# Kernel tuning notes

Hardware: AMD Instinct MI355X
Metric: run time of the kernel (lower is better)

The kernel has to match this reference:

```python
import jax, jax.numpy as jnp
import numpy as np

N = 16384      # total nodes (hits)
K = 8          # n_neighbors
NB = 8         # number of graphs in batch
IN_C = 6       # in_channels
HID = 128      # hidden_channels
NCLS = 3       # num_classes
SLOPE = 0.2    # GATv2 leaky_relu negative_slope
BIG = 1e30     # mask value for cross-graph pairs


def setup_inputs() -> dict:
    key = jax.random.key(0)
    ks = jax.random.split(key, 32)
    coord = jax.random.normal(ks[0], (N, 3), dtype=jnp.float32)
    feat = jax.random.normal(ks[1], (N, IN_C), dtype=jnp.float32)
    batch = jnp.sort(jax.random.randint(ks[2], (N,), 0, NB)).astype(jnp.int32)

    def lin_w(k, fan_in, fan_out):
        return (jax.random.normal(k, (fan_in, fan_out), dtype=jnp.float32)
                * np.float32(1.0 / np.sqrt(fan_in)))

    inp = {"coord": coord, "feat": feat, "batch": batch}
    dims = [IN_C, HID, HID]  # input dim of each of the 3 GATv2 layers
    kidx = 3
    for l, din in enumerate(dims):
        inp[f"Wl{l}"] = lin_w(ks[kidx], din, HID); kidx += 1
        inp[f"bl{l}"] = jnp.zeros((HID,), jnp.float32)
        inp[f"Wr{l}"] = lin_w(ks[kidx], din, HID); kidx += 1
        inp[f"br{l}"] = jnp.zeros((HID,), jnp.float32)
        inp[f"att{l}"] = (jax.random.normal(ks[kidx], (HID,), dtype=jnp.float32)
                          * np.float32(1.0 / np.sqrt(HID))); kidx += 1
        inp[f"bias{l}"] = jnp.zeros((HID,), jnp.float32)
    inp["Wf"] = lin_w(ks[kidx], HID, NCLS)
    inp["bf"] = jnp.zeros((NCLS,), jnp.float32)
    return inp


def knn_idx(coord, batch):
    # pairwise squared distances, masked so neighbors stay within the same graph
    d2 = jnp.sum((coord[:, None, :] - coord[None, :, :]) ** 2, axis=-1)  # [N,N]
    d2 = jnp.where(batch[:, None] == batch[None, :], d2, BIG)
    _, idx = jax.lax.top_k(-d2, K)  # [N,K] nearest (includes self at dist 0)
    return idx


def gatv2_layer(x, idx, Wl, bl, Wr, br, att, bias):
    xl = x @ Wl + bl                         # [N,H] source transform
    xr = x @ Wr + br                         # [N,H] target transform
    g = xl[idx]                              # [N,K,H] gather neighbor features
    e = jax.nn.leaky_relu(g + xr[:, None, :], SLOPE)
    logits = e @ att                         # [N,K] attention scores
    alpha = jax.nn.softmax(logits, axis=1)   # softmax over each node's K nbrs
    return jnp.einsum('nk,nkh->nh', alpha, g) + bias


def reference(coord, feat, batch,
              Wl0, bl0, Wr0, br0, att0, bias0,
              Wl1, bl1, Wr1, br1, att1, bias1,
              Wl2, bl2, Wr2, br2, att2, bias2,
              Wf, bf):
    idx = knn_idx(coord, batch)
    x = jax.nn.relu(gatv2_layer(feat, idx, Wl0, bl0, Wr0, br0, att0, bias0))
    x = jax.nn.relu(gatv2_layer(x, idx, Wl1, bl1, Wr1, br1, att1, bias1))
    x = jax.nn.relu(gatv2_layer(x, idx, Wl2, bl2, Wr2, br2, att2, bias2))
    return x @ Wf + bf
```

## Files before the change

### kernel.cpp

```cpp
#include <hip/hip_runtime.h>
#include <hip/hip_bf16.h>
#include <float.h>
#include <limits.h>

#define NNODES 16384
#define KNB 8
#define HIDC 128
#define KNN_CAP 2560

__device__ __forceinline__ float wave_sum(float x) {
  x += __int_as_float(__builtin_amdgcn_update_dpp(0, __float_as_int(x), 0xB1, 0xF, 0xF, true));
  x += __int_as_float(__builtin_amdgcn_update_dpp(0, __float_as_int(x), 0x4E, 0xF, 0xF, true));
  x += __int_as_float(__builtin_amdgcn_update_dpp(0, __float_as_int(x), 0x124, 0xF, 0xF, true));
  x += __int_as_float(__builtin_amdgcn_update_dpp(0, __float_as_int(x), 0x128, 0xF, 0xF, true));
  float r0 = __int_as_float(__builtin_amdgcn_readlane(__float_as_int(x), 0));
  float r1 = __int_as_float(__builtin_amdgcn_readlane(__float_as_int(x), 16));
  float r2 = __int_as_float(__builtin_amdgcn_readlane(__float_as_int(x), 32));
  float r3 = __int_as_float(__builtin_amdgcn_readlane(__float_as_int(x), 48));
  return (r0 + r1) + (r2 + r3);
}

__device__ __forceinline__ float wave_min_f32(float x) {
  x = fminf(x, __int_as_float(__builtin_amdgcn_update_dpp(0, __float_as_int(x), 0xB1, 0xF, 0xF, true)));
  x = fminf(x, __int_as_float(__builtin_amdgcn_update_dpp(0, __float_as_int(x), 0x4E, 0xF, 0xF, true)));
  x = fminf(x, __int_as_float(__builtin_amdgcn_update_dpp(0, __float_as_int(x), 0x124, 0xF, 0xF, true)));
  x = fminf(x, __int_as_float(__builtin_amdgcn_update_dpp(0, __float_as_int(x), 0x128, 0xF, 0xF, true)));
  float r0 = __int_as_float(__builtin_amdgcn_readlane(__float_as_int(x), 0));
  float r1 = __int_as_float(__builtin_amdgcn_readlane(__float_as_int(x), 16));
  float r2 = __int_as_float(__builtin_amdgcn_readlane(__float_as_int(x), 32));
  float r3 = __int_as_float(__builtin_amdgcn_readlane(__float_as_int(x), 48));
  return fminf(fminf(r0, r1), fminf(r2, r3));
}

__device__ __forceinline__ float dist2(float ax, float ay, float az,
                                       float bx, float by, float bz) {
  float dx = ax - bx, dy = ay - by, dz = az - bz;
  return fmaf(dz, dz, fmaf(dy, dy, dx * dx));
}

#define INS8(d)                                   \
  do {                                            \
    float _d = (d);                               \
    l7 = __builtin_amdgcn_fmed3f(_d, l6, l7);     \
    l6 = __builtin_amdgcn_fmed3f(_d, l5, l6);     \
    l5 = __builtin_amdgcn_fmed3f(_d, l4, l5);     \
    l4 = __builtin_amdgcn_fmed3f(_d, l3, l4);     \
    l3 = __builtin_amdgcn_fmed3f(_d, l2, l3);     \
    l2 = __builtin_amdgcn_fmed3f(_d, l1, l2);     \
    l1 = __builtin_amdgcn_fmed3f(_d, l0, l1);     \
    l0 = fminf(l0, _d);                           \
  } while (0)

__global__ void seg_kernel(const int* __restrict__ batch, int* __restrict__ seg) {
  int b = threadIdx.x;
  if (b > 8) return;
  int lo = 0, hi = NNODES;
  while (lo < hi) { int m = (lo + hi) >> 1; if (batch[m] < b) lo = m + 1; else hi = m; }
  seg[b] = lo;
}

__global__ __launch_bounds__(512) void knn_kernel(
    const float* __restrict__ coord, const int* __restrict__ batch,
    const int* __restrict__ seg, int* __restrict__ knn) {
  __shared__ float4 tile[KNN_CAP];
  int t = threadIdx.x;
  int lane = t & 63;
  int n0 = blockIdx.x * 8;
  int n = n0 + (t >> 6);

  int b0 = batch[n0], b7 = batch[n0 + 7], bw = batch[n];
  int smin = seg[b0];
  int emax = seg[b7 + 1];
  int s_w = seg[bw];
  int e_w = seg[bw + 1];
  int win_end = min(emax, smin + KNN_CAP);
  int cnt_fill = win_end - smin;

  for (int i = t; i < cnt_fill; i += 512) {
    const float* cp = coord + (size_t)(smin + i) * 3;
    tile[i] = make_float4(cp[0], cp[1], cp[2], 0.f);
  }
  __syncthreads();

  float cx = coord[n*3+0], cy = coord[n*3+1], cz = coord[n*3+2];

  float l0 = FLT_MAX, l1 = FLT_MAX, l2 = FLT_MAX, l3 = FLT_MAX,
        l4 = FLT_MAX, l5 = FLT_MAX, l6 = FLT_MAX, l7 = FLT_MAX;
  int lo_i = s_w - smin;
  int hi_i = min(e_w, win_end) - smin;
  #pragma unroll 2
  for (int base = lo_i; base < hi_i; base += 64) {
    int i = base + lane;
    bool ok = i < hi_i;
    float4 c = tile[ok ? i : lo_i];
    float d = dist2(c.x, c.y, c.z, cx, cy, cz);
    d = ok ? d : FLT_MAX;
    INS8(d);
  }
  for (int base = max(s_w, win_end); base < e_w; base += 64) {
    int j = base + lane;
    bool ok = j < e_w;
    int jc = ok ? j : s_w;
    float d = dist2(coord[jc*3+0], coord[jc*3+1], coord[jc*3+2], cx, cy, cz);
    d = ok ? d : FLT_MAX;
    INS8(d);
  }

  float T = 0.f;
  #pragma unroll
  for (int r = 0; r < KNB; ++r) {
    float m = wave_min_f32(l0);
    T = m;
    unsigned long long msk = __ballot(l0 == m);
    int p = (int)__builtin_ctzll(msk);
    if (lane == p) {
      l0 = l1; l1 = l2; l2 = l3; l3 = l4; l4 = l5; l5 = l6; l6 = l7; l7 = FLT_MAX;
    }
  }

  int cnt = 0;
  for (int base = lo_i; base < hi_i; base += 64) {
    int i = base + lane;
    bool ok = i < hi_i;
    float4 c = tile[ok ? i : lo_i];
    float d = dist2(c.x, c.y, c.z, cx, cy, cz);
    bool win = ok && (d <= T);
    unsigned long long msk = __ballot(win);
    if (msk) {
      int rank = __popcll(msk & ((1ull << lane) - 1ull));
      int slot = cnt + rank;
      if (win && slot < KNB) knn[n*KNB + slot] = smin + i;
      cnt += __popcll(msk);
    }
  }
  for (int base = max(s_w, win_end); base < e_w; base += 64) {
    int j = base + lane;
    bool ok = j < e_w;
    int jc = ok ? j : s_w;
    float d = dist2(coord[jc*3+0], coord[jc*3+1], coord[jc*3+2], cx, cy, cz);
    bool win = ok && (d <= T);
    unsigned long long msk = __ballot(win);
    if (msk) {
      int rank = __popcll(msk & ((1ull << lane) - 1ull));
      int slot = cnt + rank;
      if (win && slot < KNB) knn[n*KNB + slot] = j;
      cnt += __popcll(msk);
    }
  }
}

template<int K>
__global__ __launch_bounds__(256) void lin2_kernel(
    const float* __restrict__ x,
    const float* __restrict__ Wl, const float* __restrict__ bl,
    const float* __restrict__ Wr, const float* __restrict__ br,
    float* __restrict__ xl, float* __restrict__ xr) {
  __shared__ float xs[32 * K];
  int t = threadIdx.x;
  int node0 = blockIdx.x * 32;
  for (int i = t; i < 32 * K; i += 256) xs[i] = x[node0 * K + i];
  __syncthreads();
  int cg = t & 63;
  int ng = t >> 6;
  int c0 = cg * 4;
  bool isR = (c0 >= HIDC);
  const float* W    = isR ? Wr : Wl;
  const float* bias = isR ? br : bl;
  float* dst        = isR ? xr : xl;
  int wc = isR ? (c0 - HIDC) : c0;

  float4 acc[8];
  #pragma unroll
  for (int nn = 0; nn < 8; ++nn) acc[nn] = make_float4(0.f, 0.f, 0.f, 0.f);

  if constexpr (K % 4 == 0) {
    for (int k0 = 0; k0 < K; k0 += 4) {
      float4 xv[8];
      #pragma unroll
      for (int nn = 0; nn < 8; ++nn)
        xv[nn] = *(const float4*)&xs[(ng * 8 + nn) * K + k0];
      #pragma unroll
      for (int q = 0; q < 4; ++q) {
        float4 w = *(const float4*)(W + (size_t)(k0 + q) * HIDC + wc);
        #pragma unroll
        for (int nn = 0; nn < 8; ++nn) {
          float xq = (q == 0) ? xv[nn].x : (q == 1) ? xv[nn].y : (q == 2) ? xv[nn].z : xv[nn].w;
          acc[nn].x = fmaf(xq, w.x, acc[nn].x);
          acc[nn].y = fmaf(xq, w.y, acc[nn].y);
          acc[nn].z = fmaf(xq, w.z, acc[nn].z);
          acc[nn].w = fmaf(xq, w.w, acc[nn].w);
        }
      }
    }
  } else {
    for (int k = 0; k < K; ++k) {
      float4 w = *(const float4*)(W + (size_t)k * HIDC + wc);
      #pragma unroll
      for (int nn = 0; nn < 8; ++nn) {
        float xq = xs[(ng * 8 + nn) * K + k];
        acc[nn].x = fmaf(xq, w.x, acc[nn].x);
        acc[nn].y = fmaf(xq, w.y, acc[nn].y);
        acc[nn].z = fmaf(xq, w.z, acc[nn].z);
        acc[nn].w = fmaf(xq, w.w, acc[nn].w);
      }
    }
  }
  float4 b4 = *(const float4*)(bias + wc);
  #pragma unroll
  for (int nn = 0; nn < 8; ++nn) {
    int node = node0 + ng * 8 + nn;
    float4 o;
    o.x = acc[nn].x + b4.x; o.y = acc[nn].y + b4.y;
    o.z = acc[nn].z + b4.z; o.w = acc[nn].w + b4.w;
    *(float4*)(dst + (size_t)node * HIDC + wc) = o;
  }
}

template<bool FINAL>
__global__ __launch_bounds__(256) void gat_attn_kernel(
    const float* __restrict__ xl, const float* __restrict__ xr,
    const int* __restrict__ knn, const float* __restrict__ att,
    const float* __restrict__ bias, float* __restrict__ xout,
    const float* __restrict__ Wf, const float* __restrict__ bf,
    float* __restrict__ out) {
  int wid = threadIdx.x >> 6;
  int lane = threadIdx.x & 63;
  int n = blockIdx.x * 4 + wid;
  int c0 = 2 * lane, c1 = 2 * lane + 1;
  float2 xr2 = *(const float2*)(xr + (size_t)n * HIDC + c0);
  float2 a2  = *(const float2*)(att + c0);
  int myj = (lane < KNB) ? knn[n * KNB + lane] : 0;
  float g0[8], g1[8], lg[8];
  #pragma unroll
  for (int k = 0; k < 8; ++k) {
    int j = __builtin_amdgcn_readlane(myj, k);
    float2 g = *(const float2*)(xl + (size_t)j * HIDC + c0);
    g0[k] = g.x; g1[k] = g.y;
    float e0 = g.x + xr2.x; e0 = (e0 > 0.f) ? e0 : 0.2f * e0;
    float e1 = g.y + xr2.y; e1 = (e1 > 0.f) ? e1 : 0.2f * e1;
    lg[k] = wave_sum(e0 * a2.x + e1 * a2.y);
  }
  float mx = lg[0];
  #pragma unroll
  for (int k = 1; k < 8; ++k) mx = fmaxf(mx, lg[k]);
  float ssum = 0.f, w[8];
  #pragma unroll
  for (int k = 0; k < 8; ++k) { w[k] = __expf(lg[k] - mx); ssum += w[k]; }
  float inv = 1.f / ssum;
  float o0 = 0.f, o1 = 0.f;
  #pragma unroll
  for (int k = 0; k < 8; ++k) { o0 += w[k] * g0[k]; o1 += w[k] * g1[k]; }
  o0 = fmaxf(fmaf(o0, inv, bias[c0]), 0.f);
  o1 = fmaxf(fmaf(o1, inv, bias[c1]), 0.f);
  if (!FINAL) {
    float2 o; o.x = o0; o.y = o1;
    *(float2*)(xout + (size_t)n * HIDC + c0) = o;
  } else {
    #pragma unroll
    for (int cls = 0; cls < 3; ++cls) {
      float p = wave_sum(o0 * Wf[c0 * 3 + cls] + o1 * Wf[c1 * 3 + cls]);
      if (lane == 0) out[n * 3 + cls] = p + bf[cls];
    }
  }
}

extern "C" void kernel_launch(void* const* d_in, const int* in_sizes, int n_in,
                              void* d_out, int out_size, void* d_ws, size_t ws_size,
                              hipStream_t stream) {
  const float* coord = (const float*)d_in[0];
  const float* feat  = (const float*)d_in[1];
  const int*   batch = (const int*)d_in[2];
  const float* Wl0 = (const float*)d_in[3];
  const float* bl0 = (const float*)d_in[4];
  const float* Wr0 = (const float*)d_in[5];
  const float* br0 = (const float*)d_in[6];
  const float* att0  = (const float*)d_in[7];
  const float* bias0 = (const float*)d_in[8];
  const float* Wl1 = (const float*)d_in[9];
  const float* bl1 = (const float*)d_in[10];
  const float* Wr1 = (const float*)d_in[11];
  const float* br1 = (const float*)d_in[12];
  const float* att1  = (const float*)d_in[13];
  const float* bias1 = (const float*)d_in[14];
  const float* Wl2 = (const float*)d_in[15];
  const float* bl2 = (const float*)d_in[16];
  const float* Wr2 = (const float*)d_in[17];
  const float* br2 = (const float*)d_in[18];
  const float* att2  = (const float*)d_in[19];
  const float* bias2 = (const float*)d_in[20];
  const float* Wf = (const float*)d_in[21];
  const float* bf = (const float*)d_in[22];
  float* out = (float*)d_out;

  char* ws = (char*)d_ws;
  int*   knn = (int*)ws;
  float* xl  = (float*)(ws + (512 << 10));
  float* xr  = xl + (size_t)NNODES * HIDC;
  float* xb0 = xr + (size_t)NNODES * HIDC;
  float* xb1 = xb0 + (size_t)NNODES * HIDC;
  int*   seg = (int*)xb0;

  seg_kernel<<<1, 16, 0, stream>>>(batch, seg);
  knn_kernel<<<NNODES / 8, 512, 0, stream>>>(coord, batch, seg, knn);

  lin2_kernel<6><<<NNODES / 32, 256, 0, stream>>>(feat, Wl0, bl0, Wr0, br0, xl, xr);
  gat_attn_kernel<false><<<NNODES / 4, 256, 0, stream>>>(xl, xr, knn, att0, bias0, xb0,
                                                         nullptr, nullptr, nullptr);

  lin2_kernel<128><<<NNODES / 32, 256, 0, stream>>>(xb0, Wl1, bl1, Wr1, br1, xl, xr);
  gat_attn_kernel<false><<<NNODES / 4, 256, 0, stream>>>(xl, xr, knn, att1, bias1, xb1,
                                                         nullptr, nullptr, nullptr);

  lin2_kernel<128><<<NNODES / 32, 256, 0, stream>>>(xb1, Wl2, bl2, Wr2, br2, xl, xr);
  gat_attn_kernel<true><<<NNODES / 4, 256, 0, stream>>>(xl, xr, knn, att2, bias2, nullptr,
                                                        Wf, bf, out);
}
```

Measured before the change: 152.7 us.

## Fuse segment search, kNN and first linear layer; process two queries per wave

```diff
diff --git a/kernel.cpp b/kernel.cpp
--- a/kernel.cpp
+++ b/kernel.cpp
@@ -6,7 +6,7 @@
 #define NNODES 16384
 #define KNB 8
 #define HIDC 128
-#define KNN_CAP 2560
+#define KNN_CAP 2528
 
 __device__ __forceinline__ float wave_sum(float x) {
   x += __int_as_float(__builtin_amdgcn_update_dpp(0, __float_as_int(x), 0xB1, 0xF, 0xF, true));
@@ -38,74 +38,21 @@
   return fmaf(dz, dz, fmaf(dy, dy, dx * dx));
 }
 
-#define INS8(d)                                   \
-  do {                                            \
-    float _d = (d);                               \
-    l7 = __builtin_amdgcn_fmed3f(_d, l6, l7);     \
-    l6 = __builtin_amdgcn_fmed3f(_d, l5, l6);     \
-    l5 = __builtin_amdgcn_fmed3f(_d, l4, l5);     \
-    l4 = __builtin_amdgcn_fmed3f(_d, l3, l4);     \
-    l3 = __builtin_amdgcn_fmed3f(_d, l2, l3);     \
-    l2 = __builtin_amdgcn_fmed3f(_d, l1, l2);     \
-    l1 = __builtin_amdgcn_fmed3f(_d, l0, l1);     \
-    l0 = fminf(l0, _d);                           \
+#define INS8V(_d, a0, a1, a2, a3, a4, a5, a6, a7)  \
+  do {                                             \
+    a7 = __builtin_amdgcn_fmed3f(_d, a6, a7);      \
+    a6 = __builtin_amdgcn_fmed3f(_d, a5, a6);      \
+    a5 = __builtin_amdgcn_fmed3f(_d, a4, a5);      \
+    a4 = __builtin_amdgcn_fmed3f(_d, a3, a4);      \
+    a3 = __builtin_amdgcn_fmed3f(_d, a2, a3);      \
+    a2 = __builtin_amdgcn_fmed3f(_d, a1, a2);      \
+    a1 = __builtin_amdgcn_fmed3f(_d, a0, a1);      \
+    a0 = fminf(a0, _d);                            \
   } while (0)
 
-__global__ void seg_kernel(const int* __restrict__ batch, int* __restrict__ seg) {
-  int b = threadIdx.x;
-  if (b > 8) return;
-  int lo = 0, hi = NNODES;
-  while (lo < hi) { int m = (lo + hi) >> 1; if (batch[m] < b) lo = m + 1; else hi = m; }
-  seg[b] = lo;
-}
-
-__global__ __launch_bounds__(512) void knn_kernel(
-    const float* __restrict__ coord, const int* __restrict__ batch,
-    const int* __restrict__ seg, int* __restrict__ knn) {
-  __shared__ float4 tile[KNN_CAP];
-  int t = threadIdx.x;
-  int lane = t & 63;
-  int n0 = blockIdx.x * 8;
-  int n = n0 + (t >> 6);
-
-  int b0 = batch[n0], b7 = batch[n0 + 7], bw = batch[n];
-  int smin = seg[b0];
-  int emax = seg[b7 + 1];
-  int s_w = seg[bw];
-  int e_w = seg[bw + 1];
-  int win_end = min(emax, smin + KNN_CAP);
-  int cnt_fill = win_end - smin;
-
-  for (int i = t; i < cnt_fill; i += 512) {
-    const float* cp = coord + (size_t)(smin + i) * 3;
-    tile[i] = make_float4(cp[0], cp[1], cp[2], 0.f);
-  }
-  __syncthreads();
-
-  float cx = coord[n*3+0], cy = coord[n*3+1], cz = coord[n*3+2];
-
-  float l0 = FLT_MAX, l1 = FLT_MAX, l2 = FLT_MAX, l3 = FLT_MAX,
-        l4 = FLT_MAX, l5 = FLT_MAX, l6 = FLT_MAX, l7 = FLT_MAX;
-  int lo_i = s_w - smin;
-  int hi_i = min(e_w, win_end) - smin;
-  #pragma unroll 2
-  for (int base = lo_i; base < hi_i; base += 64) {
-    int i = base + lane;
-    bool ok = i < hi_i;
-    float4 c = tile[ok ? i : lo_i];
-    float d = dist2(c.x, c.y, c.z, cx, cy, cz);
-    d = ok ? d : FLT_MAX;
-    INS8(d);
-  }
-  for (int base = max(s_w, win_end); base < e_w; base += 64) {
-    int j = base + lane;
-    bool ok = j < e_w;
-    int jc = ok ? j : s_w;
-    float d = dist2(coord[jc*3+0], coord[jc*3+1], coord[jc*3+2], cx, cy, cz);
-    d = ok ? d : FLT_MAX;
-    INS8(d);
-  }
-
+__device__ __forceinline__ float merge_T(float l0, float l1, float l2, float l3,
+                                         float l4, float l5, float l6, float l7,
+                                         int lane) {
   float T = 0.f;
   #pragma unroll
   for (int r = 0; r < KNB; ++r) {
@@ -113,38 +60,204 @@
     T = m;
     unsigned long long msk = __ballot(l0 == m);
     int p = (int)__builtin_ctzll(msk);
-    if (lane == p) {
-      l0 = l1; l1 = l2; l2 = l3; l3 = l4; l4 = l5; l5 = l6; l6 = l7; l7 = FLT_MAX;
-    }
-  }
-
+    if (lane == p) { l0 = l1; l1 = l2; l2 = l3; l3 = l4; l4 = l5; l5 = l6; l6 = l7; l7 = FLT_MAX; }
+  }
+  return T;
+}
+
+__device__ void knn_global_single(const float* __restrict__ coord,
+                                  float qx, float qy, float qz,
+                                  int s, int e, int lane,
+                                  int* __restrict__ knn_row) {
+  float l0 = FLT_MAX, l1 = FLT_MAX, l2 = FLT_MAX, l3 = FLT_MAX,
+        l4 = FLT_MAX, l5 = FLT_MAX, l6 = FLT_MAX, l7 = FLT_MAX;
+  for (int base = s; base < e; base += 64) {
+    int j = base + lane;
+    bool ok = j < e;
+    int jc = ok ? j : s;
+    float d = dist2(coord[jc*3+0], coord[jc*3+1], coord[jc*3+2], qx, qy, qz);
+    d = ok ? d : FLT_MAX;
+    INS8V(d, l0, l1, l2, l3, l4, l5, l6, l7);
+  }
+  float T = merge_T(l0, l1, l2, l3, l4, l5, l6, l7, lane);
+  unsigned long long lt = (1ull << lane) - 1ull;
   int cnt = 0;
-  for (int base = lo_i; base < hi_i; base += 64) {
-    int i = base + lane;
-    bool ok = i < hi_i;
-    float4 c = tile[ok ? i : lo_i];
-    float d = dist2(c.x, c.y, c.z, cx, cy, cz);
+  for (int base = s; base < e; base += 64) {
+    int j = base + lane;
+    bool ok = j < e;
+    int jc = ok ? j : s;
+    float d = dist2(coord[jc*3+0], coord[jc*3+1], coord[jc*3+2], qx, qy, qz);
     bool win = ok && (d <= T);
     unsigned long long msk = __ballot(win);
     if (msk) {
-      int rank = __popcll(msk & ((1ull << lane) - 1ull));
-      int slot = cnt + rank;
-      if (win && slot < KNB) knn[n*KNB + slot] = smin + i;
+      int slot = cnt + __popcll(msk & lt);
+      if (win && slot < KNB) knn_row[slot] = j;
       cnt += __popcll(msk);
     }
   }
-  for (int base = max(s_w, win_end); base < e_w; base += 64) {
-    int j = base + lane;
-    bool ok = j < e_w;
-    int jc = ok ? j : s_w;
-    float d = dist2(coord[jc*3+0], coord[jc*3+1], coord[jc*3+2], cx, cy, cz);
-    bool win = ok && (d <= T);
-    unsigned long long msk = __ballot(win);
-    if (msk) {
-      int rank = __popcll(msk & ((1ull << lane) - 1ull));
-      int slot = cnt + rank;
-      if (win && slot < KNB) knn[n*KNB + slot] = j;
-      cnt += __popcll(msk);
+}
+
+__global__ __launch_bounds__(512) void knnlin_kernel(
+    const float* __restrict__ coord, const int* __restrict__ batch,
+    const float* __restrict__ feat,
+    const float* __restrict__ Wl0, const float* __restrict__ bl0,
+    const float* __restrict__ Wr0, const float* __restrict__ br0,
+    int* __restrict__ knn, float* __restrict__ xl, float* __restrict__ xr) {
+  __shared__ float4 tile[KNN_CAP];
+  __shared__ int segs[9];
+  int t = threadIdx.x;
+  int lane = t & 63;
+  int wid = t >> 6;
+  int n0 = blockIdx.x * 16;
+
+  if (t < 9) {
+    int lo = 0, hi = NNODES;
+    while (lo < hi) { int m = (lo + hi) >> 1; if (batch[m] < t) lo = m + 1; else hi = m; }
+    segs[t] = lo;
+  }
+  __syncthreads();
+
+  int b0 = batch[n0];
+  int blast = batch[n0 + 15];
+  int smin = segs[b0];
+  int emax = segs[blast + 1];
+  int win_end = min(emax, smin + KNN_CAP);
+  int cnt_fill = win_end - smin;
+
+  for (int i = t; i < cnt_fill; i += 512) {
+    const float* cp = coord + (size_t)(smin + i) * 3;
+    tile[i] = make_float4(cp[0], cp[1], cp[2], 0.f);
+  }
+  __syncthreads();
+
+  int nA = n0 + wid * 2, nB = nA + 1;
+  int bA = batch[nA], bB = batch[nB];
+  int sA = segs[bA], eA = segs[bA + 1];
+  bool fast = (bA == bB) && (eA - smin <= KNN_CAP);
+
+  float ax = coord[nA*3+0], ay = coord[nA*3+1], az = coord[nA*3+2];
+  float bx = coord[nB*3+0], by = coord[nB*3+1], bz = coord[nB*3+2];
+
+  if (fast) {
+    int lo_i = sA - smin;
+    int M = eA - sA;
+    int F = M >> 6, R = M & 63;
+
+    float a0 = FLT_MAX, a1 = FLT_MAX, a2 = FLT_MAX, a3 = FLT_MAX,
+          a4 = FLT_MAX, a5 = FLT_MAX, a6 = FLT_MAX, a7 = FLT_MAX;
+    float b0r = FLT_MAX, b1 = FLT_MAX, b2 = FLT_MAX, b3 = FLT_MAX,
+          b4 = FLT_MAX, b5 = FLT_MAX, b6 = FLT_MAX, b7 = FLT_MAX;
+    const float4* tl = tile + lo_i;
+    #pragma unroll 4
+    for (int it = 0; it < F; ++it) {
+      float4 c = tl[lane];
+      tl += 64;
+      float dA = dist2(c.x, c.y, c.z, ax, ay, az);
+      float dB = dist2(c.x, c.y, c.z, bx, by, bz);
+      INS8V(dA, a0, a1, a2, a3, a4, a5, a6, a7);
+      INS8V(dB, b0r, b1, b2, b3, b4, b5, b6, b7);
+    }
+    if (R) {
+      int i = lo_i + F * 64 + lane;
+      bool ok = (F * 64 + lane) < M;
+      float4 c = tile[ok ? i : lo_i];
+      float dA = dist2(c.x, c.y, c.z, ax, ay, az);
+      float dB = dist2(c.x, c.y, c.z, bx, by, bz);
+      dA = ok ? dA : FLT_MAX;
+      dB = ok ? dB : FLT_MAX;
+      INS8V(dA, a0, a1, a2, a3, a4, a5, a6, a7);
+      INS8V(dB, b0r, b1, b2, b3, b4, b5, b6, b7);
+    }
+
+    float TA = merge_T(a0, a1, a2, a3, a4, a5, a6, a7, lane);
+    float TB = merge_T(b0r, b1, b2, b3, b4, b5, b6, b7, lane);
+
+    unsigned long long lt = (1ull << lane) - 1ull;
+    int cntA = 0, cntB = 0;
+    const float4* tl2 = tile + lo_i;
+    for (int it = 0; it < F; ++it) {
+      float4 c = tl2[lane];
+      tl2 += 64;
+      float dA = dist2(c.x, c.y, c.z, ax, ay, az);
+      float dB = dist2(c.x, c.y, c.z, bx, by, bz);
+      int gidx = sA + it * 64 + lane;
+      unsigned long long mA = __ballot(dA <= TA);
+      if (mA) {
+        int slot = cntA + __popcll(mA & lt);
+        if ((dA <= TA) && slot < KNB) knn[nA*KNB + slot] = gidx;
+        cntA += __popcll(mA);
+      }
+      unsigned long long mB = __ballot(dB <= TB);
+      if (mB) {
+        int slot = cntB + __popcll(mB & lt);
+        if ((dB <= TB) && slot < KNB) knn[nB*KNB + slot] = gidx;
+        cntB += __popcll(mB);
+      }
+    }
+    if (R) {
+      int li = F * 64 + lane;
+      bool ok = li < M;
+      float4 c = tile[ok ? (lo_i + li) : lo_i];
+      float dA = dist2(c.x, c.y, c.z, ax, ay, az);
+      float dB = dist2(c.x, c.y, c.z, bx, by, bz);
+      int gidx = sA + li;
+      bool wA = ok && (dA <= TA);
+      bool wB = ok && (dB <= TB);
+      unsigned long long mA = __ballot(wA);
+      if (mA) {
+        int slot = cntA + __popcll(mA & lt);
+        if (wA && slot < KNB) knn[nA*KNB + slot] = gidx;
+        cntA += __popcll(mA);
+      }
+      unsigned long long mB = __ballot(wB);
+      if (mB) {
+        int slot = cntB + __popcll(mB & lt);
+        if (wB && slot < KNB) knn[nB*KNB + slot] = gidx;
+        cntB += __popcll(mB);
+      }
+    }
+  } else {
+    int sB2 = segs[bB], eB2 = segs[bB + 1];
+    knn_global_single(coord, ax, ay, az, sA, eA, lane, knn + (size_t)nA * KNB);
+    knn_global_single(coord, bx, by, bz, sB2, eB2, lane, knn + (size_t)nB * KNB);
+  }
+
+  {
+    int cg = t & 63;
+    bool isR = cg >= 32;
+    const float* W  = isR ? Wr0 : Wl0;
+    const float* bi = isR ? br0 : bl0;
+    float* dst      = isR ? xr : xl;
+    int wc = (cg & 31) * 4;
+    float4 w0 = *(const float4*)(W + 0 * HIDC + wc);
+    float4 w1 = *(const float4*)(W + 1 * HIDC + wc);
+    float4 w2 = *(const float4*)(W + 2 * HIDC + wc);
+    float4 w3 = *(const float4*)(W + 3 * HIDC + wc);
+    float4 w4 = *(const float4*)(W + 4 * HIDC + wc);
+    float4 w5 = *(const float4*)(W + 5 * HIDC + wc);
+    float4 bb = *(const float4*)(bi + wc);
+    #pragma unroll
+    for (int s2 = 0; s2 < 2; ++s2) {
+      int node = n0 + wid * 2 + s2;
+      const float* fr = feat + (size_t)node * 6;
+      float f0 = fr[0], f1 = fr[1], f2 = fr[2], f3 = fr[3], f4 = fr[4], f5 = fr[5];
+      float4 acc = make_float4(0.f, 0.f, 0.f, 0.f);
+      acc.x = fmaf(f0, w0.x, acc.x); acc.y = fmaf(f0, w0.y, acc.y);
+      acc.z = fmaf(f0, w0.z, acc.z); acc.w = fmaf(f0, w0.w, acc.w);
+      acc.x = fmaf(f1, w1.x, acc.x); acc.y = fmaf(f1, w1.y, acc.y);
+      acc.z = fmaf(f1, w1.z, acc.z); acc.w = fmaf(f1, w1.w, acc.w);
+      acc.x = fmaf(f2, w2.x, acc.x); acc.y = fmaf(f2, w2.y, acc.y);
+      acc.z = fmaf(f2, w2.z, acc.z); acc.w = fmaf(f2, w2.w, acc.w);
+      acc.x = fmaf(f3, w3.x, acc.x); acc.y = fmaf(f3, w3.y, acc.y);
+      acc.z = fmaf(f3, w3.z, acc.z); acc.w = fmaf(f3, w3.w, acc.w);
+      acc.x = fmaf(f4, w4.x, acc.x); acc.y = fmaf(f4, w4.y, acc.y);
+      acc.z = fmaf(f4, w4.z, acc.z); acc.w = fmaf(f4, w4.w, acc.w);
+      acc.x = fmaf(f5, w5.x, acc.x); acc.y = fmaf(f5, w5.y, acc.y);
+      acc.z = fmaf(f5, w5.z, acc.z); acc.w = fmaf(f5, w5.w, acc.w);
+      float4 o;
+      o.x = acc.x + bb.x; o.y = acc.y + bb.y;
+      o.z = acc.z + bb.z; o.w = acc.w + bb.w;
+      *(float4*)(dst + (size_t)node * HIDC + wc) = o;
     }
   }
 }
@@ -173,31 +286,17 @@
   #pragma unroll
   for (int nn = 0; nn < 8; ++nn) acc[nn] = make_float4(0.f, 0.f, 0.f, 0.f);
 
-  if constexpr (K % 4 == 0) {
-    for (int k0 = 0; k0 < K; k0 += 4) {
-      float4 xv[8];
-      #pragma unroll
-      for (int nn = 0; nn < 8; ++nn)
-        xv[nn] = *(const float4*)&xs[(ng * 8 + nn) * K + k0];
-      #pragma unroll
-      for (int q = 0; q < 4; ++q) {
-        float4 w = *(const float4*)(W + (size_t)(k0 + q) * HIDC + wc);
-        #pragma unroll
-        for (int nn = 0; nn < 8; ++nn) {
-          float xq = (q == 0) ? xv[nn].x : (q == 1) ? xv[nn].y : (q == 2) ? xv[nn].z : xv[nn].w;
-          acc[nn].x = fmaf(xq, w.x, acc[nn].x);
-          acc[nn].y = fmaf(xq, w.y, acc[nn].y);
-          acc[nn].z = fmaf(xq, w.z, acc[nn].z);
-          acc[nn].w = fmaf(xq, w.w, acc[nn].w);
-        }
-      }
-    }
-  } else {
-    for (int k = 0; k < K; ++k) {
-      float4 w = *(const float4*)(W + (size_t)k * HIDC + wc);
+  for (int k0 = 0; k0 < K; k0 += 4) {
+    float4 xv[8];
+    #pragma unroll
+    for (int nn = 0; nn < 8; ++nn)
+      xv[nn] = *(const float4*)&xs[(ng * 8 + nn) * K + k0];
+    #pragma unroll
+    for (int q = 0; q < 4; ++q) {
+      float4 w = *(const float4*)(W + (size_t)(k0 + q) * HIDC + wc);
       #pragma unroll
       for (int nn = 0; nn < 8; ++nn) {
-        float xq = xs[(ng * 8 + nn) * K + k];
+        float xq = (q == 0) ? xv[nn].x : (q == 1) ? xv[nn].y : (q == 2) ? xv[nn].z : xv[nn].w;
         acc[nn].x = fmaf(xq, w.x, acc[nn].x);
         acc[nn].y = fmaf(xq, w.y, acc[nn].y);
         acc[nn].z = fmaf(xq, w.z, acc[nn].z);
@@ -298,12 +397,9 @@
   float* xr  = xl + (size_t)NNODES * HIDC;
   float* xb0 = xr + (size_t)NNODES * HIDC;
   float* xb1 = xb0 + (size_t)NNODES * HIDC;
-  int*   seg = (int*)xb0;
-
-  seg_kernel<<<1, 16, 0, stream>>>(batch, seg);
-  knn_kernel<<<NNODES / 8, 512, 0, stream>>>(coord, batch, seg, knn);
-
-  lin2_kernel<6><<<NNODES / 32, 256, 0, stream>>>(feat, Wl0, bl0, Wr0, br0, xl, xr);
+
+  knnlin_kernel<<<NNODES / 16, 512, 0, stream>>>(coord, batch, feat,
+                                                 Wl0, bl0, Wr0, br0, knn, xl, xr);
   gat_attn_kernel<false><<<NNODES / 4, 256, 0, stream>>>(xl, xr, knn, att0, bias0, xb0,
                                                          nullptr, nullptr, nullptr);
 
```

New measurement: 144.6 us. 5.3% less time.
